# Optimization experiments

Measured on AMD Instinct MI355X. Metric: run time of the kernel, lower is better.

The kernel has to match this reference:

```python
import jax, jax.numpy as jnp
import numpy as np

N_HEAD = 16
NEG = -10000.0


def setup_inputs() -> dict:
    key = jax.random.key(0)
    k1, k2, k3 = jax.random.split(key, 3)
    B, S, NX = 2, 2048, 1024
    x = jax.random.normal(k1, (B, S, NX), dtype=jnp.float32)
    # Conv1D weights: y = x @ W + b (HF Conv1D stores weight as [in, out])
    w_attn = jax.random.normal(k2, (NX, 3 * NX), dtype=jnp.float32) * 0.02
    b_attn = jnp.zeros((3 * NX,), dtype=jnp.float32)
    w_proj = jax.random.normal(k3, (NX, NX), dtype=jnp.float32) * 0.02
    b_proj = jnp.zeros((NX,), dtype=jnp.float32)
    return {"x": x, "w_attn": w_attn, "b_attn": b_attn,
            "w_proj": w_proj, "b_proj": b_proj}


def reference(x, w_attn, b_attn, w_proj, b_proj):
    B, S, NX = x.shape
    H = N_HEAD
    D = NX // H  # head dim
    qkv = x @ w_attn + b_attn                      # [B, S, 3*NX]
    q, k, v = jnp.split(qkv, 3, axis=-1)
    # split heads -> [B, H, S, D]
    q = q.reshape(B, S, H, D).transpose(0, 2, 1, 3)
    k = k.reshape(B, S, H, D).transpose(0, 2, 1, 3)
    v = v.reshape(B, S, H, D).transpose(0, 2, 1, 3)
    # scores [B, H, S, S], scaled (scale=True)
    w = jnp.einsum('bhqd,bhkd->bhqk', q, k) / jnp.sqrt(jnp.asarray(D, x.dtype))
    # causal additive mask exactly as the torch code: w*b + NEG*(1-b)
    bias = jnp.tril(jnp.ones((S, S), dtype=x.dtype))[None, None]  # [1,1,S,S]
    w = w * bias + NEG * (1.0 - bias)
    w = jax.nn.softmax(w, axis=-1)
    a = jnp.einsum('bhqk,bhkd->bhqd', w, v)        # [B, H, S, D]
    a = a.transpose(0, 2, 1, 3).reshape(B, S, NX)  # merge heads
    return a @ w_proj + b_proj
```

## Files before the change

### kernel.cpp

```cpp
#include <hip/hip_runtime.h>
#include <cstdint>
#include <cstddef>


typedef __bf16 bf16;
typedef __bf16 bf16x8 __attribute__((ext_vector_type(8)));
typedef __bf16 bf16x4 __attribute__((ext_vector_type(4)));
typedef float f32x4 __attribute__((ext_vector_type(4)));

#define MFMA16(a, b, c) __builtin_amdgcn_mfma_f32_16x16x32_bf16(a, b, c, 0, 0, 0)

typedef const __attribute__((address_space(1))) void* gas_ptr;
typedef __attribute__((address_space(3))) void* las_ptr;
__device__ __forceinline__ void async16(const void* g, void* l) {
    __builtin_amdgcn_global_load_lds((gas_ptr)g, (las_ptr)l, 16, 0, 0);
}
__device__ __forceinline__ float exp2f_fast(float x) { return __builtin_amdgcn_exp2f(x); }

__global__ __launch_bounds__(256) void prep_kernel(const float* __restrict__ x, bf16* __restrict__ xb,
                                                   const float* __restrict__ wa, bf16* __restrict__ wTa,
                                                   const float* __restrict__ wp, bf16* __restrict__ wTp) {
    __shared__ float tile[32][33];
    const int bid = blockIdx.x, tid = threadIdx.x;
    if (bid < 4096) {
        int i = (bid * 256 + tid) * 4;
        float4 v = *reinterpret_cast<const float4*>(x + i);
        bf16x4 o;
        o[0] = (bf16)v.x; o[1] = (bf16)v.y; o[2] = (bf16)v.z; o[3] = (bf16)v.w;
        *reinterpret_cast<bf16x4*>(xb + i) = o;
        return;
    }
    const float* in; bf16* out; int N, t;
    if (bid < 7168) { t = bid - 4096; in = wa; out = wTa; N = 3072; }
    else            { t = bid - 7168; in = wp; out = wTp; N = 1024; }
    const int K = 1024;
    int bx = t % (N >> 5), by = t / (N >> 5);
    int n0 = bx * 32, k0 = by * 32, tx = tid & 31, ty = tid >> 5;
#pragma unroll
    for (int i = 0; i < 32; i += 8)
        tile[ty + i][tx] = in[(size_t)(k0 + ty + i) * N + n0 + tx];
    __syncthreads();
#pragma unroll
    for (int i = 0; i < 32; i += 8)
        out[(size_t)(n0 + ty + i) * K + k0 + tx] = (bf16)tile[tx][ty + i];
}

template <int OUT_BF16>
__global__ __launch_bounds__(256) void gemm_kernel(const bf16* __restrict__ A,
                                                   const bf16* __restrict__ Bt,
                                                   const float* __restrict__ bias,
                                                   void* __restrict__ Cout,
                                                   int M, int N, int K) {
    __shared__ bf16 Alds[2][128 * 32];
    __shared__ bf16 Blds[2][128 * 32];
    const int tid = threadIdx.x;
    const int w = tid >> 6, l = tid & 63;
    const int lane16 = l & 15, quad = l >> 4;
    const int wr = w >> 1, wc = w & 1;
    const int row0 = blockIdx.y * 128, col0 = blockIdx.x * 128;

    const int e = tid * 8;
    const int sr = e >> 5, sc = e & 31;

    f32x4 zero4 = {0.f, 0.f, 0.f, 0.f};
    f32x4 acc[4][4];
#pragma unroll
    for (int i = 0; i < 4; ++i)
#pragma unroll
        for (int j = 0; j < 4; ++j) acc[i][j] = zero4;

#pragma unroll
    for (int ch = 0; ch < 2; ++ch) {
        async16(A + (size_t)(row0 + ch * 64 + sr) * K + sc, &Alds[0][ch * 2048 + e]);
        async16(Bt + (size_t)(col0 + ch * 64 + sr) * K + sc, &Blds[0][ch * 2048 + e]);
    }

    const int niter = K >> 5;
    for (int it = 0; it < niter; ++it) {
        const int cur = it & 1;
        __syncthreads();
        if (it + 1 < niter) {
            const int k1 = (it + 1) << 5;
#pragma unroll
            for (int ch = 0; ch < 2; ++ch) {
                async16(A + (size_t)(row0 + ch * 64 + sr) * K + k1 + sc, &Alds[cur ^ 1][ch * 2048 + e]);
                async16(Bt + (size_t)(col0 + ch * 64 + sr) * K + k1 + sc, &Blds[cur ^ 1][ch * 2048 + e]);
            }
        }
        bf16x8 af[4], bfr[4];
#pragma unroll
        for (int i = 0; i < 4; ++i) {
            af[i] = *reinterpret_cast<const bf16x8*>(&Alds[cur][(64 * wr + 16 * i + lane16) * 32 + quad * 8]);
            bfr[i] = *reinterpret_cast<const bf16x8*>(&Blds[cur][(64 * wc + 16 * i + lane16) * 32 + quad * 8]);
        }
#pragma unroll
        for (int i = 0; i < 4; ++i)
#pragma unroll
            for (int j = 0; j < 4; ++j) acc[i][j] = MFMA16(af[i], bfr[j], acc[i][j]);
    }

#pragma unroll
    for (int i = 0; i < 4; ++i)
#pragma unroll
        for (int j = 0; j < 4; ++j)
#pragma unroll
            for (int r = 0; r < 4; ++r) {
                int row = row0 + 64 * wr + 16 * i + quad * 4 + r;
                int col = col0 + 64 * wc + 16 * j + lane16;
                float v = acc[i][j][r] + bias[col];
                if (OUT_BF16)
                    reinterpret_cast<bf16*>(Cout)[(size_t)row * N + col] = (bf16)v;
                else
                    reinterpret_cast<float*>(Cout)[(size_t)row * N + col] = v;
            }
}

template <int OUT_BF16>
__global__ __launch_bounds__(256) void gemm64k_kernel(const bf16* __restrict__ A,
                                                      const bf16* __restrict__ Bt,
                                                      const float* __restrict__ bias,
                                                      void* __restrict__ Cout,
                                                      int M, int N, int K) {
    __shared__ bf16 Alds[2][64 * 64];
    __shared__ bf16 Blds[2][128 * 64];
    const int tid = threadIdx.x;
    const int w = tid >> 6, l = tid & 63;
    const int lane16 = l & 15, quad = l >> 4;
    const int wr = w >> 1, wc = w & 1;
    const int row0 = blockIdx.y * 64, col0 = blockIdx.x * 128;

    f32x4 zero4 = {0.f, 0.f, 0.f, 0.f};
    f32x4 acc[2][4];
#pragma unroll
    for (int i = 0; i < 2; ++i)
#pragma unroll
        for (int j = 0; j < 4; ++j) acc[i][j] = zero4;

    auto stage = [&](int buf, int k0) {
#pragma unroll
        for (int c = 0; c < 2; ++c) {
            int idx = c * 256 + tid;
            int r = idx >> 3, cc = idx & 7, gc = cc ^ (r & 7);
            async16(A + (size_t)(row0 + r) * K + k0 + gc * 8, &Alds[buf][idx * 8]);
        }
#pragma unroll
        for (int c = 0; c < 4; ++c) {
            int idx = c * 256 + tid;
            int r = idx >> 3, cc = idx & 7, gc = cc ^ (r & 7);
            async16(Bt + (size_t)(col0 + r) * K + k0 + gc * 8, &Blds[buf][idx * 8]);
        }
    };

    stage(0, 0);
    const int niter = K >> 6;
    for (int it = 0; it < niter; ++it) {
        const int cur = it & 1;
        __syncthreads();
        if (it + 1 < niter) stage(cur ^ 1, (it + 1) << 6);
        bf16x8 af[2][2], bfr[4][2];
#pragma unroll
        for (int i = 0; i < 2; ++i) {
            int r = 32 * wr + 16 * i + lane16;
#pragma unroll
            for (int ks = 0; ks < 2; ++ks) {
                int cc = (quad + 4 * ks) ^ (r & 7);
                af[i][ks] = *reinterpret_cast<const bf16x8*>(&Alds[cur][r * 64 + cc * 8]);
            }
        }
#pragma unroll
        for (int j = 0; j < 4; ++j) {
            int r = 64 * wc + 16 * j + lane16;
#pragma unroll
            for (int ks = 0; ks < 2; ++ks) {
                int cc = (quad + 4 * ks) ^ (r & 7);
                bfr[j][ks] = *reinterpret_cast<const bf16x8*>(&Blds[cur][r * 64 + cc * 8]);
            }
        }
#pragma unroll
        for (int ks = 0; ks < 2; ++ks)
#pragma unroll
            for (int i = 0; i < 2; ++i)
#pragma unroll
                for (int j = 0; j < 4; ++j) acc[i][j] = MFMA16(af[i][ks], bfr[j][ks], acc[i][j]);
    }

#pragma unroll
    for (int i = 0; i < 2; ++i)
#pragma unroll
        for (int j = 0; j < 4; ++j)
#pragma unroll
            for (int r = 0; r < 4; ++r) {
                int row = row0 + 32 * wr + 16 * i + quad * 4 + r;
                int col = col0 + 64 * wc + 16 * j + lane16;
                float v = acc[i][j][r] + bias[col];
                if (OUT_BF16)
                    reinterpret_cast<bf16*>(Cout)[(size_t)row * N + col] = (bf16)v;
                else
                    reinterpret_cast<float*>(Cout)[(size_t)row * N + col] = v;
            }
}

__global__ __launch_bounds__(256) void attn_kernel(const bf16* __restrict__ qkv,
                                                   bf16* __restrict__ aout) {
    const int S = 2048;
    const int bh = blockIdx.x;
    const int b = bh >> 4, h = bh & 15;
    const int rr = blockIdx.y >> 3, j = blockIdx.y & 7;
    const int qt = (rr == 0) ? (31 - j) : (rr == 1) ? (16 + j) : (rr == 2) ? (15 - j) : j;
    const int nkt = qt + 1;
    const int tid = threadIdx.x, w = tid >> 6, l = tid & 63;
    const int lane16 = l & 15, quad = l >> 4;

    __shared__ bf16 Klds[64 * 72];
    __shared__ bf16 Vt[64 * 72];
    __shared__ bf16 Plds[4][16 * 72];

    const bf16* base = qkv + (size_t)b * S * 3072;
    const float qscale = 0.125f * 1.4426950408889634f;
    const float NEGs = -10000.0f * 1.4426950408889634f;

    bf16x8 qf[2];
#pragma unroll
    for (int hv = 0; hv < 2; ++hv) {
        const bf16* qp = base + (size_t)(qt * 64 + 16 * w + lane16) * 3072 + h * 64;
        bf16x8 t = *reinterpret_cast<const bf16x8*>(qp + hv * 32 + quad * 8);
#pragma unroll
        for (int jj = 0; jj < 8; ++jj) t[jj] = (bf16)((float)t[jj] * qscale);
        qf[hv] = t;
    }

    f32x4 zero4 = {0.f, 0.f, 0.f, 0.f};
    f32x4 o[4];
#pragma unroll
    for (int df = 0; df < 4; ++df) o[df] = zero4;
    float lsum = 0.f;

    const int kr = tid >> 3, kc = (tid & 7) * 8;
    const int vp = tid & 31, vd = (tid >> 5) * 8;
    bf16x8 kreg0, kreg1, vreg0, vreg1;
    auto load_tile = [&](int kt) {
        const bf16* tb = base + (size_t)(kt * 64) * 3072;
        kreg0 = *reinterpret_cast<const bf16x8*>(tb + (size_t)kr * 3072 + 1024 + h * 64 + kc);
        kreg1 = *reinterpret_cast<const bf16x8*>(tb + (size_t)(32 + kr) * 3072 + 1024 + h * 64 + kc);
        vreg0 = *reinterpret_cast<const bf16x8*>(tb + (size_t)(2 * vp) * 3072 + 2048 + h * 64 + vd);
        vreg1 = *reinterpret_cast<const bf16x8*>(tb + (size_t)(2 * vp + 1) * 3072 + 2048 + h * 64 + vd);
    };

    load_tile(0);
    for (int kt = 0; kt < nkt; ++kt) {
        __syncthreads();
        *reinterpret_cast<bf16x8*>(&Klds[kr * 72 + kc]) = kreg0;
        *reinterpret_cast<bf16x8*>(&Klds[(32 + kr) * 72 + kc]) = kreg1;
#pragma unroll
        for (int jj = 0; jj < 8; ++jj) {
            union { bf16 h2[2]; uint32_t u; } pk;
            pk.h2[0] = vreg0[jj]; pk.h2[1] = vreg1[jj];
            *reinterpret_cast<uint32_t*>(&Vt[(vd + jj) * 72 + 2 * vp]) = pk.u;
        }
        __syncthreads();
        if (kt + 1 < nkt) load_tile(kt + 1);

        f32x4 st[4];
#pragma unroll
        for (int kf = 0; kf < 4; ++kf) {
            bf16x8 k0 = *reinterpret_cast<const bf16x8*>(&Klds[(kf * 16 + lane16) * 72 + quad * 8]);
            bf16x8 k1 = *reinterpret_cast<const bf16x8*>(&Klds[(kf * 16 + lane16) * 72 + 32 + quad * 8]);
            f32x4 z = zero4;
            z = MFMA16(k0, qf[0], z);
            z = MFMA16(k1, qf[1], z);
            st[kf] = z;
        }

        if (kt == qt) {
            const int q = qt * 64 + 16 * w + lane16;
#pragma unroll
            for (int kf = 0; kf < 4; ++kf)
#pragma unroll
                for (int r = 0; r < 4; ++r)
                    if (kt * 64 + kf * 16 + quad * 4 + r > q) st[kf][r] = NEGs;
        }

        float rs = 0.f;
        bf16* Prow = &Plds[w][lane16 * 72];
#pragma unroll
        for (int kf = 0; kf < 4; ++kf) {
            bf16x4 pk;
#pragma unroll
            for (int r = 0; r < 4; ++r) {
                float pv = exp2f_fast(st[kf][r]);
                rs += pv;
                pk[r] = (bf16)pv;
            }
            *reinterpret_cast<bf16x4*>(Prow + kf * 16 + quad * 4) = pk;
        }
        lsum += rs;

#pragma unroll
        for (int kf2 = 0; kf2 < 2; ++kf2) {
            bf16x8 pf = *reinterpret_cast<const bf16x8*>(
                &Plds[w][lane16 * 72 + kf2 * 32 + quad * 8]);
#pragma unroll
            for (int df = 0; df < 4; ++df) {
                bf16x8 vf = *reinterpret_cast<const bf16x8*>(
                    &Vt[(df * 16 + lane16) * 72 + kf2 * 32 + quad * 8]);
                o[df] = MFMA16(pf, vf, o[df]);
            }
        }
    }

    lsum += __shfl_xor(lsum, 16, 64);
    lsum += __shfl_xor(lsum, 32, 64);
    float inv = 1.0f / lsum;

#pragma unroll
    for (int r = 0; r < 4; ++r) {
        float li = __shfl(inv, quad * 4 + r, 64);
        int row = qt * 64 + 16 * w + quad * 4 + r;
#pragma unroll
        for (int df = 0; df < 4; ++df)
            aout[(size_t)(b * S + row) * 1024 + h * 64 + df * 16 + lane16] =
                (bf16)(o[df][r] * li);
    }
}

extern "C" void kernel_launch(void* const* d_in, const int* in_sizes, int n_in,
                              void* d_out, int out_size, void* d_ws, size_t ws_size,
                              hipStream_t stream) {
    const float* x      = (const float*)d_in[0];
    const float* w_attn = (const float*)d_in[1];
    const float* b_attn = (const float*)d_in[2];
    const float* w_proj = (const float*)d_in[3];
    const float* b_proj = (const float*)d_in[4];
    float* out = (float*)d_out;
    char* ws = (char*)d_ws;

    const int Mtok = 4096, NX = 1024, N3 = 3072;
    bf16* xb   = (bf16*)(ws);
    bf16* wTa  = (bf16*)(ws + ((size_t)8 << 20));
    bf16* wTp  = (bf16*)(ws + ((size_t)14 << 20));
    bf16* qkv  = (bf16*)(ws + ((size_t)16 << 20));
    bf16* abuf = (bf16*)(ws + ((size_t)40 << 20));

    prep_kernel<<<dim3(8192), 256, 0, stream>>>(x, xb, w_attn, wTa, w_proj, wTp);
    gemm_kernel<1><<<dim3(N3 / 128, Mtok / 128), 256, 0, stream>>>(xb, wTa, b_attn, qkv, Mtok, N3, NX);
    attn_kernel<<<dim3(32, 32), 256, 0, stream>>>(qkv, abuf);
    gemm64k_kernel<0><<<dim3(NX / 128, Mtok / 64), 256, 0, stream>>>(abuf, wTp, b_proj, out, Mtok, NX, NX);
}
```

Baseline: 171.0 us.

## Split attention keys across waves and keep P in registers

The attention kernel now gives each wave a 16-key slice of every key tile across all 64 query rows, instead of 16 query rows across all keys. The softmax probabilities are fed straight from registers into a 16x16x16 MFMA, so the per-wave LDS round trip for P goes away. The cost is a cross-wave reduction of the output accumulators and row sums through shared memory at the end. The kernel also holds 4x more accumulator registers and gets a launch-bounds occupancy hint of 3.

```diff
diff --git a/kernel.cpp b/kernel.cpp
--- a/kernel.cpp
+++ b/kernel.cpp
@@ -6,9 +6,11 @@
 typedef __bf16 bf16;
 typedef __bf16 bf16x8 __attribute__((ext_vector_type(8)));
 typedef __bf16 bf16x4 __attribute__((ext_vector_type(4)));
+typedef short s16x4 __attribute__((ext_vector_type(4)));
 typedef float f32x4 __attribute__((ext_vector_type(4)));
 
 #define MFMA16(a, b, c) __builtin_amdgcn_mfma_f32_16x16x32_bf16(a, b, c, 0, 0, 0)
+#define MFMA16K16(a, b, c) __builtin_amdgcn_mfma_f32_16x16x16bf16_1k(a, b, c, 0, 0, 0)
 
 typedef const __attribute__((address_space(1))) void* gas_ptr;
 typedef __attribute__((address_space(3))) void* las_ptr;
@@ -200,40 +202,47 @@
             }
 }
 
-__global__ __launch_bounds__(256) void attn_kernel(const bf16* __restrict__ qkv,
-                                                   bf16* __restrict__ aout) {
+__global__ __launch_bounds__(256, 3) void attn_kernel(const bf16* __restrict__ qkv,
+                                                      bf16* __restrict__ aout) {
     const int S = 2048;
     const int bh = blockIdx.x;
     const int b = bh >> 4, h = bh & 15;
-    const int rr = blockIdx.y >> 3, j = blockIdx.y & 7;
-    const int qt = (rr == 0) ? (31 - j) : (rr == 1) ? (16 + j) : (rr == 2) ? (15 - j) : j;
+    const int rr = blockIdx.y >> 3, jj = blockIdx.y & 7;
+    const int qt = (rr == 0) ? (31 - jj) : (rr == 1) ? (16 + jj) : (rr == 2) ? (15 - jj) : jj;
     const int nkt = qt + 1;
     const int tid = threadIdx.x, w = tid >> 6, l = tid & 63;
     const int lane16 = l & 15, quad = l >> 4;
 
-    __shared__ bf16 Klds[64 * 72];
-    __shared__ bf16 Vt[64 * 72];
-    __shared__ bf16 Plds[4][16 * 72];
+    __shared__ __align__(16) char smem[64 * 72 * 2 * 2];
+    bf16* Klds = (bf16*)smem;
+    bf16* Vt = (bf16*)(smem + 64 * 72 * 2);
+    float* Ored = (float*)smem;
+    __shared__ float Lred[4][4][16];
 
     const bf16* base = qkv + (size_t)b * S * 3072;
     const float qscale = 0.125f * 1.4426950408889634f;
     const float NEGs = -10000.0f * 1.4426950408889634f;
 
-    bf16x8 qf[2];
-#pragma unroll
-    for (int hv = 0; hv < 2; ++hv) {
-        const bf16* qp = base + (size_t)(qt * 64 + 16 * w + lane16) * 3072 + h * 64;
-        bf16x8 t = *reinterpret_cast<const bf16x8*>(qp + hv * 32 + quad * 8);
-#pragma unroll
-        for (int jj = 0; jj < 8; ++jj) t[jj] = (bf16)((float)t[jj] * qscale);
-        qf[hv] = t;
+    bf16x8 qf[4][2];
+#pragma unroll
+    for (int q4 = 0; q4 < 4; ++q4) {
+        const bf16* qp = base + (size_t)(qt * 64 + 16 * q4 + lane16) * 3072 + h * 64;
+#pragma unroll
+        for (int dh = 0; dh < 2; ++dh) {
+            bf16x8 t = *reinterpret_cast<const bf16x8*>(qp + dh * 32 + quad * 8);
+#pragma unroll
+            for (int j = 0; j < 8; ++j) t[j] = (bf16)((float)t[j] * qscale);
+            qf[q4][dh] = t;
+        }
     }
 
     f32x4 zero4 = {0.f, 0.f, 0.f, 0.f};
-    f32x4 o[4];
-#pragma unroll
-    for (int df = 0; df < 4; ++df) o[df] = zero4;
-    float lsum = 0.f;
+    f32x4 o[4][4];
+#pragma unroll
+    for (int i = 0; i < 4; ++i)
+#pragma unroll
+        for (int j = 0; j < 4; ++j) o[i][j] = zero4;
+    float lsum[4] = {0.f, 0.f, 0.f, 0.f};
 
     const int kr = tid >> 3, kc = (tid & 7) * 8;
     const int vp = tid & 31, vd = (tid >> 5) * 8;
@@ -252,74 +261,96 @@
         *reinterpret_cast<bf16x8*>(&Klds[kr * 72 + kc]) = kreg0;
         *reinterpret_cast<bf16x8*>(&Klds[(32 + kr) * 72 + kc]) = kreg1;
 #pragma unroll
-        for (int jj = 0; jj < 8; ++jj) {
+        for (int j = 0; j < 8; ++j) {
             union { bf16 h2[2]; uint32_t u; } pk;
-            pk.h2[0] = vreg0[jj]; pk.h2[1] = vreg1[jj];
-            *reinterpret_cast<uint32_t*>(&Vt[(vd + jj) * 72 + 2 * vp]) = pk.u;
+            pk.h2[0] = vreg0[j]; pk.h2[1] = vreg1[j];
+            *reinterpret_cast<uint32_t*>(&Vt[(vd + j) * 72 + 2 * vp]) = pk.u;
         }
         __syncthreads();
         if (kt + 1 < nkt) load_tile(kt + 1);
 
+        bf16x8 ka0 = *reinterpret_cast<const bf16x8*>(&Klds[(16 * w + lane16) * 72 + quad * 8]);
+        bf16x8 ka1 = *reinterpret_cast<const bf16x8*>(&Klds[(16 * w + lane16) * 72 + 32 + quad * 8]);
         f32x4 st[4];
 #pragma unroll
-        for (int kf = 0; kf < 4; ++kf) {
-            bf16x8 k0 = *reinterpret_cast<const bf16x8*>(&Klds[(kf * 16 + lane16) * 72 + quad * 8]);
-            bf16x8 k1 = *reinterpret_cast<const bf16x8*>(&Klds[(kf * 16 + lane16) * 72 + 32 + quad * 8]);
+        for (int q4 = 0; q4 < 4; ++q4) {
             f32x4 z = zero4;
-            z = MFMA16(k0, qf[0], z);
-            z = MFMA16(k1, qf[1], z);
-            st[kf] = z;
+            z = MFMA16(ka0, qf[q4][0], z);
+            z = MFMA16(ka1, qf[q4][1], z);
+            st[q4] = z;
         }
 
         if (kt == qt) {
-            const int q = qt * 64 + 16 * w + lane16;
-#pragma unroll
-            for (int kf = 0; kf < 4; ++kf)
+            const int key0 = kt * 64 + 16 * w + quad * 4;
+#pragma unroll
+            for (int q4 = 0; q4 < 4; ++q4) {
+                const int q = qt * 64 + 16 * q4 + lane16;
 #pragma unroll
                 for (int r = 0; r < 4; ++r)
-                    if (kt * 64 + kf * 16 + quad * 4 + r > q) st[kf][r] = NEGs;
-        }
-
-        float rs = 0.f;
-        bf16* Prow = &Plds[w][lane16 * 72];
-#pragma unroll
-        for (int kf = 0; kf < 4; ++kf) {
-            bf16x4 pk;
+                    if (key0 + r > q) st[q4][r] = NEGs;
+            }
+        }
+
+        s16x4 pA[4];
+#pragma unroll
+        for (int q4 = 0; q4 < 4; ++q4) {
+            union { bf16 b[4]; s16x4 s; } pk;
+            float rs = 0.f;
 #pragma unroll
             for (int r = 0; r < 4; ++r) {
-                float pv = exp2f_fast(st[kf][r]);
+                float pv = exp2f_fast(st[q4][r]);
                 rs += pv;
-                pk[r] = (bf16)pv;
-            }
-            *reinterpret_cast<bf16x4*>(Prow + kf * 16 + quad * 4) = pk;
-        }
-        lsum += rs;
-
-#pragma unroll
-        for (int kf2 = 0; kf2 < 2; ++kf2) {
-            bf16x8 pf = *reinterpret_cast<const bf16x8*>(
-                &Plds[w][lane16 * 72 + kf2 * 32 + quad * 8]);
-#pragma unroll
-            for (int df = 0; df < 4; ++df) {
-                bf16x8 vf = *reinterpret_cast<const bf16x8*>(
-                    &Vt[(df * 16 + lane16) * 72 + kf2 * 32 + quad * 8]);
-                o[df] = MFMA16(pf, vf, o[df]);
-            }
-        }
-    }
-
-    lsum += __shfl_xor(lsum, 16, 64);
-    lsum += __shfl_xor(lsum, 32, 64);
-    float inv = 1.0f / lsum;
-
-#pragma unroll
-    for (int r = 0; r < 4; ++r) {
-        float li = __shfl(inv, quad * 4 + r, 64);
-        int row = qt * 64 + 16 * w + quad * 4 + r;
-#pragma unroll
-        for (int df = 0; df < 4; ++df)
-            aout[(size_t)(b * S + row) * 1024 + h * 64 + df * 16 + lane16] =
-                (bf16)(o[df][r] * li);
+                pk.b[r] = (bf16)pv;
+            }
+            lsum[q4] += rs;
+            pA[q4] = pk.s;
+        }
+
+#pragma unroll
+        for (int df = 0; df < 4; ++df) {
+            s16x4 vB = *reinterpret_cast<const s16x4*>(&Vt[(df * 16 + lane16) * 72 + 16 * w + quad * 4]);
+#pragma unroll
+            for (int q4 = 0; q4 < 4; ++q4)
+                o[q4][df] = MFMA16K16(pA[q4], vB, o[q4][df]);
+        }
+    }
+
+#pragma unroll
+    for (int q4 = 0; q4 < 4; ++q4) {
+        float lw = lsum[q4];
+        lw += __shfl_xor(lw, 16, 64);
+        lw += __shfl_xor(lw, 32, 64);
+        lsum[q4] = lw;
+    }
+    if (quad == 0) {
+#pragma unroll
+        for (int q4 = 0; q4 < 4; ++q4) Lred[w][q4][lane16] = lsum[q4];
+    }
+    __syncthreads();
+    float invw = Lred[0][w][lane16] + Lred[1][w][lane16] + Lred[2][w][lane16] + Lred[3][w][lane16];
+    invw = 1.0f / invw;
+    float invq[4];
+#pragma unroll
+    for (int r = 0; r < 4; ++r) invq[r] = __shfl(invw, quad * 4 + r, 64);
+
+#pragma unroll
+    for (int df = 0; df < 4; ++df) {
+        __syncthreads();
+#pragma unroll
+        for (int q4 = 0; q4 < 4; ++q4)
+#pragma unroll
+            for (int r = 0; r < 4; ++r)
+                Ored[(w * 64 + 16 * q4 + 4 * quad + r) * 17 + lane16] = o[q4][df][r];
+        __syncthreads();
+#pragma unroll
+        for (int r = 0; r < 4; ++r) {
+            int qrow = 16 * w + 4 * quad + r;
+            float s = Ored[(0 * 64 + qrow) * 17 + lane16] + Ored[(1 * 64 + qrow) * 17 + lane16] +
+                      Ored[(2 * 64 + qrow) * 17 + lane16] + Ored[(3 * 64 + qrow) * 17 + lane16];
+            int row = qt * 64 + qrow;
+            aout[(size_t)(b * S + row) * 1024 + h * 64 + 16 * df + lane16] =
+                (bf16)(s * invq[r]);
+        }
     }
 }
 
```

After: 173.4 us. No clear change (+1.4%).
